# Performance work log

Hardware: AMD Instinct MI355X
Metric: run time of the kernel (lower is better)

The kernel has to match this reference:

```python
import jax, jax.numpy as jnp
import numpy as np
import math

D_MODEL = 1024
N_HEADS = 16
D_K = D_MODEL // N_HEADS


def setup_inputs() -> dict:
    key = jax.random.key(0)
    ks = jax.random.split(key, 12)
    B, S, D = 4, 2048, D_MODEL
    scale = 1.0 / math.sqrt(D)
    inp = {
        "q": jax.random.normal(ks[0], (B, S, D), jnp.float32),
        "k": jax.random.normal(ks[1], (B, S, D), jnp.float32),
        "v": jax.random.normal(ks[2], (B, S, D), jnp.float32),
        "w_q": jax.random.normal(ks[3], (D, D), jnp.float32) * scale,
        "b_q": jnp.zeros((D,), jnp.float32),
        "w_k": jax.random.normal(ks[4], (D, D), jnp.float32) * scale,
        "b_k": jnp.zeros((D,), jnp.float32),
        "w_v": jax.random.normal(ks[5], (D, D), jnp.float32) * scale,
        "b_v": jnp.zeros((D,), jnp.float32),
        "w_o": jax.random.normal(ks[6], (D, D), jnp.float32) * scale,
        "b_o": jnp.zeros((D,), jnp.float32),
        "ln_gamma": jnp.ones((D,), jnp.float32),
        "ln_beta": jnp.zeros((D,), jnp.float32),
    }
    return inp


def reference(q, k, v, w_q, b_q, w_k, b_k, w_v, b_v, w_o, b_o, ln_gamma, ln_beta):
    B, Sq, D = q.shape
    Sk = k.shape[1]
    residual = q
    # Projections (torch Linear: x @ W.T + b); split into heads -> [B, H, S, d_k]
    qh = (q @ w_q.T + b_q).reshape(B, Sq, N_HEADS, D_K).transpose(0, 2, 1, 3)
    kh = (k @ w_k.T + b_k).reshape(B, Sk, N_HEADS, D_K).transpose(0, 2, 1, 3)
    vh = (v @ w_v.T + b_v).reshape(B, Sk, N_HEADS, D_K).transpose(0, 2, 1, 3)
    # Scaled dot-product attention (dropout is identity in eval mode)
    scores = jnp.einsum("bhqd,bhkd->bhqk", qh, kh) / jnp.sqrt(jnp.float32(D_K))
    attn = jax.nn.softmax(scores, axis=-1)  # [B, H, Sq, Sk]
    ctx = jnp.einsum("bhqk,bhkd->bhqd", attn, vh)
    ctx = ctx.transpose(0, 2, 1, 3).reshape(B, Sq, D)
    out = ctx @ w_o.T + b_o
    # Post-LN with residual
    x = out + residual
    mu = jnp.mean(x, axis=-1, keepdims=True)
    var = jnp.var(x, axis=-1, keepdims=True)
    out = (x - mu) / jnp.sqrt(var + 1e-5) * ln_gamma + ln_beta
    return out, attn
```

## Files before the change

kernel.cpp:

```cpp
#include <hip/hip_runtime.h>

#define B_ 4
#define S_ 2048
#define D_ 1024
#define H_ 16
#define DK_ 64
#define M_ (B_ * S_)

typedef __attribute__((ext_vector_type(8))) _Float16 f16x8;
typedef __attribute__((ext_vector_type(4))) _Float16 f16x4;
typedef __attribute__((ext_vector_type(4))) float f32x4;

#define QSCALE 0.18033688011113607f

__device__ __forceinline__ f32x4 mfma16(f16x8 a, f16x8 b, f32x4 c) {
  return __builtin_amdgcn_mfma_f32_16x16x32_f16(a, b, c, 0, 0, 0);
}

__device__ __forceinline__ void gl2lds(const _Float16* g, _Float16* l) {
  __builtin_amdgcn_global_load_lds(
      (const __attribute__((address_space(1))) void*)g,
      (__attribute__((address_space(3))) void*)l, 16, 0, 0);
}

#define NW8 (D_ * D_ / 8)
__global__ __launch_bounds__(256) void cvt_w(
    const float* __restrict__ wq, const float* __restrict__ wk,
    const float* __restrict__ wv, const float* __restrict__ wo,
    _Float16* __restrict__ wqh, _Float16* __restrict__ wkh,
    _Float16* __restrict__ wvh, _Float16* __restrict__ woh) {
  const int i = blockIdx.x * 256 + threadIdx.x;
  const int t = i >> 17;
  const int off = i & (NW8 - 1);
  const float* src = t == 0 ? wq : (t == 1 ? wk : (t == 2 ? wv : wo));
  _Float16* dst = t == 0 ? wqh : (t == 1 ? wkh : (t == 2 ? wvh : woh));
  const f32x4 a = *reinterpret_cast<const f32x4*>(&src[(size_t)off * 8]);
  const f32x4 b = *reinterpret_cast<const f32x4*>(&src[(size_t)off * 8 + 4]);
  f16x8 h;
  h[0] = (_Float16)a[0]; h[1] = (_Float16)a[1]; h[2] = (_Float16)a[2]; h[3] = (_Float16)a[3];
  h[4] = (_Float16)b[0]; h[5] = (_Float16)b[1]; h[6] = (_Float16)b[2]; h[7] = (_Float16)b[3];
  *reinterpret_cast<f16x8*>(&dst[(size_t)off * 8]) = h;
}

__global__ __launch_bounds__(256) void gemm_qkv(
    const float* __restrict__ Xq, const float* __restrict__ Xk, const float* __restrict__ Xv,
    const _Float16* __restrict__ Wq, const _Float16* __restrict__ Wk, const _Float16* __restrict__ Wv,
    const float* __restrict__ bq, const float* __restrict__ bk, const float* __restrict__ bv,
    _Float16* __restrict__ Qh, _Float16* __restrict__ Kh, _Float16* __restrict__ Vt) {
  __shared__ _Float16 As[128 * 72];
  __shared__ _Float16 Bs[128 * 64];
  const int third = blockIdx.x >> 9;
  const int bid = blockIdx.x & 511;
  const float* X = third == 0 ? Xq : (third == 1 ? Xk : Xv);
  const _Float16* Bw = third == 0 ? Wq : (third == 1 ? Wk : Wv);
  const float* bias = third == 0 ? bq : (third == 1 ? bk : bv);

  const int t = threadIdx.x;
  const int lane = t & 63;
  const int w = t >> 6;
  const int wr = w >> 1, wc = w & 1;
  const int l15 = lane & 15, g = lane >> 4;
  const int m0 = (bid & 63) * 128;
  const int n0 = (bid >> 6) * 128;

  f32x4 acc[4][4] = {};
  const int srow = lane >> 3;
  const int schk = (lane & 7) * 8;
  const int ar = t >> 4;
  const int ac = (t & 15) * 4;

  for (int kt = 0; kt < 16; ++kt) {
    const int k0 = kt * 64;
#pragma unroll
    for (int u = 0; u < 4; ++u)
      gl2lds(&Bw[(size_t)(n0 + u * 32 + w * 8 + srow) * D_ + k0 + schk], &Bs[u * 2048 + w * 512]);
#pragma unroll
    for (int rg = 0; rg < 8; ++rg) {
      const int r = rg * 16 + ar;
      const f32x4 vv = *reinterpret_cast<const f32x4*>(&X[(size_t)(m0 + r) * D_ + k0 + ac]);
      f16x4 hh;
      hh[0] = (_Float16)vv[0]; hh[1] = (_Float16)vv[1];
      hh[2] = (_Float16)vv[2]; hh[3] = (_Float16)vv[3];
      *reinterpret_cast<f16x4*>(&As[r * 72 + ac]) = hh;
    }
    __syncthreads();
#pragma unroll
    for (int kk = 0; kk < 2; ++kk) {
      f16x8 af[4], bfr[4];
#pragma unroll
      for (int m = 0; m < 4; ++m)
        af[m] = *reinterpret_cast<const f16x8*>(&As[(wr * 64 + m * 16 + l15) * 72 + kk * 32 + 8 * g]);
#pragma unroll
      for (int n = 0; n < 4; ++n)
        bfr[n] = *reinterpret_cast<const f16x8*>(&Bs[(wc * 64 + n * 16 + l15) * 64 + kk * 32 + 8 * g]);
#pragma unroll
      for (int m = 0; m < 4; ++m)
#pragma unroll
        for (int n = 0; n < 4; ++n)
          acc[m][n] = mfma16(af[m], bfr[n], acc[m][n]);
    }
    __syncthreads();
  }

  if (third < 2) {
    _Float16* Y = third == 0 ? Qh : Kh;
    const float scl = third == 0 ? QSCALE : 1.0f;
#pragma unroll
    for (int m = 0; m < 4; ++m)
#pragma unroll
      for (int n = 0; n < 4; ++n)
#pragma unroll
        for (int i = 0; i < 4; ++i) {
          const int R = m0 + wr * 64 + m * 16 + 4 * g + i;
          const int C = n0 + wc * 64 + n * 16 + l15;
          Y[(size_t)R * D_ + C] = (_Float16)((acc[m][n][i] + bias[C]) * scl);
        }
  } else {
#pragma unroll
    for (int m = 0; m < 4; ++m)
#pragma unroll
      for (int n = 0; n < 4; ++n) {
        const int R0 = m0 + wr * 64 + m * 16 + 4 * g;
        const int C = n0 + wc * 64 + n * 16 + l15;
        const int b = R0 >> 11, s0 = R0 & (S_ - 1);
        const int h = C >> 6, dk = C & (DK_ - 1);
        f16x4 hv;
#pragma unroll
        for (int i = 0; i < 4; ++i) hv[i] = (_Float16)(acc[m][n][i] + bias[C]);
        *reinterpret_cast<f16x4*>(&Vt[((size_t)((b * H_ + h) * DK_ + dk)) * S_ + s0]) = hv;
      }
  }
}

__global__ __launch_bounds__(256) void gemm_out(const _Float16* __restrict__ A,
                                                const _Float16* __restrict__ Bw,
                                                const float* __restrict__ bias,
                                                float* __restrict__ out) {
  __shared__ _Float16 As[128 * 64];
  __shared__ _Float16 Bs[128 * 64];
  const int t = threadIdx.x;
  const int lane = t & 63;
  const int w = t >> 6;
  const int wr = w >> 1, wc = w & 1;
  const int l15 = lane & 15, g = lane >> 4;
  const int m0 = (blockIdx.x & 63) * 128;
  const int n0 = (blockIdx.x >> 6) * 128;

  f32x4 acc[4][4] = {};
  const int srow = lane >> 3;
  const int schk = (lane & 7) * 8;

  for (int kt = 0; kt < 16; ++kt) {
    const int k0 = kt * 64;
#pragma unroll
    for (int u = 0; u < 4; ++u) {
      const int r = u * 32 + w * 8 + srow;
      gl2lds(&A[(size_t)(m0 + r) * D_ + k0 + schk], &As[u * 2048 + w * 512]);
      gl2lds(&Bw[(size_t)(n0 + r) * D_ + k0 + schk], &Bs[u * 2048 + w * 512]);
    }
    __syncthreads();
#pragma unroll
    for (int kk = 0; kk < 2; ++kk) {
      f16x8 af[4], bfr[4];
#pragma unroll
      for (int m = 0; m < 4; ++m)
        af[m] = *reinterpret_cast<const f16x8*>(&As[(wr * 64 + m * 16 + l15) * 64 + kk * 32 + 8 * g]);
#pragma unroll
      for (int n = 0; n < 4; ++n)
        bfr[n] = *reinterpret_cast<const f16x8*>(&Bs[(wc * 64 + n * 16 + l15) * 64 + kk * 32 + 8 * g]);
#pragma unroll
      for (int m = 0; m < 4; ++m)
#pragma unroll
        for (int n = 0; n < 4; ++n)
          acc[m][n] = mfma16(af[m], bfr[n], acc[m][n]);
    }
    __syncthreads();
  }

#pragma unroll
  for (int m = 0; m < 4; ++m)
#pragma unroll
    for (int n = 0; n < 4; ++n)
#pragma unroll
      for (int i = 0; i < 4; ++i) {
        const int R = m0 + wr * 64 + m * 16 + 4 * g + i;
        const int C = n0 + wc * 64 + n * 16 + l15;
        out[(size_t)R * D_ + C] = acc[m][n][i] + bias[C];
      }
}

__global__ __launch_bounds__(256) void attn_pass1(const _Float16* __restrict__ Qh,
                                                  const _Float16* __restrict__ Kh,
                                                  float* __restrict__ lbuf) {
  __shared__ float red[4][64];
  const int t = threadIdx.x;
  const int lane = t & 63;
  const int w = t >> 6;
  const int l15 = lane & 15, g = lane >> 4;
  const int qc = blockIdx.x & 31;
  const int bh = blockIdx.x >> 5;
  const int b = bh >> 4, h = bh & 15;
  const int q0 = qc * 64;
  const _Float16* Qp = Qh + (size_t)b * S_ * D_ + h * DK_;
  const _Float16* Kp = Kh + (size_t)b * S_ * D_ + h * DK_;

  f16x8 qa[4][2];
#pragma unroll
  for (int mr = 0; mr < 4; ++mr)
#pragma unroll
    for (int kk = 0; kk < 2; ++kk)
      qa[mr][kk] = *reinterpret_cast<const f16x8*>(&Qp[(size_t)(q0 + mr * 16 + l15) * D_ + kk * 32 + 8 * g]);

  float l[4][4] = {};
  const int cbeg = w * (S_ / 4), cend = cbeg + (S_ / 4);
  f16x8 kb0 = *reinterpret_cast<const f16x8*>(&Kp[(size_t)(cbeg + l15) * D_ + 8 * g]);
  f16x8 kb1 = *reinterpret_cast<const f16x8*>(&Kp[(size_t)(cbeg + l15) * D_ + 32 + 8 * g]);
  for (int c0 = cbeg; c0 < cend; c0 += 16) {
    const int cn = (c0 + 16 < cend) ? c0 + 16 : cbeg;
    const f16x8 nb0 = *reinterpret_cast<const f16x8*>(&Kp[(size_t)(cn + l15) * D_ + 8 * g]);
    const f16x8 nb1 = *reinterpret_cast<const f16x8*>(&Kp[(size_t)(cn + l15) * D_ + 32 + 8 * g]);
#pragma unroll
    for (int mr = 0; mr < 4; ++mr) {
      f32x4 sc = {};
      sc = mfma16(qa[mr][0], kb0, sc);
      sc = mfma16(qa[mr][1], kb1, sc);
#pragma unroll
      for (int i = 0; i < 4; ++i) l[mr][i] += exp2f(sc[i]);
    }
    kb0 = nb0; kb1 = nb1;
  }
#pragma unroll
  for (int mask = 1; mask < 16; mask <<= 1)
#pragma unroll
    for (int mr = 0; mr < 4; ++mr)
#pragma unroll
      for (int i = 0; i < 4; ++i) l[mr][i] += __shfl_xor(l[mr][i], mask, 64);
  if (l15 == 0)
#pragma unroll
    for (int mr = 0; mr < 4; ++mr)
#pragma unroll
      for (int i = 0; i < 4; ++i) red[w][mr * 16 + 4 * g + i] = l[mr][i];
  __syncthreads();
  if (t < 64)
    lbuf[(size_t)bh * S_ + q0 + t] = red[0][t] + red[1][t] + red[2][t] + red[3][t];
}

__global__ __launch_bounds__(256) void attn_pass2(const _Float16* __restrict__ Qh,
                                                  const _Float16* __restrict__ Kh,
                                                  const _Float16* __restrict__ Vt,
                                                  const float* __restrict__ lbuf,
                                                  float* __restrict__ attn,
                                                  _Float16* __restrict__ ctx) {
  __shared__ float Ps[4][32 * 36];
  const int t = threadIdx.x;
  const int lane = t & 63;
  const int w = t >> 6;
  const int l15 = lane & 15, g = lane >> 4;
  const int qc = blockIdx.x & 15;
  const int bh = blockIdx.x >> 4;
  const int b = bh >> 4, h = bh & 15;
  const int q0 = qc * 128 + w * 32;
  const _Float16* Qp = Qh + (size_t)b * S_ * D_ + h * DK_;
  const _Float16* Kp = Kh + (size_t)b * S_ * D_ + h * DK_;
  const _Float16* Vp = Vt + (size_t)bh * DK_ * S_;

  f16x8 qa[2][2];
#pragma unroll
  for (int mr = 0; mr < 2; ++mr)
#pragma unroll
    for (int kk = 0; kk < 2; ++kk)
      qa[mr][kk] = *reinterpret_cast<const f16x8*>(&Qp[(size_t)(q0 + mr * 16 + l15) * D_ + kk * 32 + 8 * g]);

  float il[2][4];
#pragma unroll
  for (int mr = 0; mr < 2; ++mr)
#pragma unroll
    for (int i = 0; i < 4; ++i)
      il[mr][i] = 1.0f / lbuf[(size_t)bh * S_ + q0 + mr * 16 + 4 * g + i];

  f32x4 accv[2][4] = {};
  float* Pw = Ps[w];
  const int sr = lane >> 3;
  const int sc4 = (lane & 7) * 4;

#pragma unroll 2
  for (int c0 = 0; c0 < S_; c0 += 32) {
#pragma unroll
    for (int ct = 0; ct < 2; ++ct) {
      const f16x8 kb0 = *reinterpret_cast<const f16x8*>(&Kp[(size_t)(c0 + ct * 16 + l15) * D_ + 8 * g]);
      const f16x8 kb1 = *reinterpret_cast<const f16x8*>(&Kp[(size_t)(c0 + ct * 16 + l15) * D_ + 32 + 8 * g]);
#pragma unroll
      for (int mr = 0; mr < 2; ++mr) {
        f32x4 sc = {};
        sc = mfma16(qa[mr][0], kb0, sc);
        sc = mfma16(qa[mr][1], kb1, sc);
#pragma unroll
        for (int i = 0; i < 4; ++i)
          Pw[(mr * 16 + 4 * g + i) * 36 + ct * 16 + l15] = exp2f(sc[i]) * il[mr][i];
      }
    }
#pragma unroll
    for (int j = 0; j < 4; ++j) {
      const int r = sr + 8 * j;
      const f32x4 pv = *reinterpret_cast<const f32x4*>(&Pw[r * 36 + sc4]);
      __builtin_nontemporal_store(pv,
          reinterpret_cast<f32x4*>(&attn[((size_t)bh * S_ + q0 + r) * S_ + c0 + sc4]));
    }
#pragma unroll
    for (int mr = 0; mr < 2; ++mr) {
      const f32x4 p0 = *reinterpret_cast<const f32x4*>(&Pw[(mr * 16 + l15) * 36 + 8 * g]);
      const f32x4 p1 = *reinterpret_cast<const f32x4*>(&Pw[(mr * 16 + l15) * 36 + 8 * g + 4]);
      f16x8 pa;
#pragma unroll
      for (int j = 0; j < 4; ++j) { pa[j] = (_Float16)p0[j]; pa[4 + j] = (_Float16)p1[j]; }
#pragma unroll
      for (int n = 0; n < 4; ++n) {
        const f16x8 vb = *reinterpret_cast<const f16x8*>(&Vp[(size_t)(n * 16 + l15) * S_ + c0 + 8 * g]);
        accv[mr][n] = mfma16(pa, vb, accv[mr][n]);
      }
    }
  }
#pragma unroll
  for (int mr = 0; mr < 2; ++mr)
#pragma unroll
    for (int n = 0; n < 4; ++n)
#pragma unroll
      for (int i = 0; i < 4; ++i) {
        const int row = q0 + mr * 16 + 4 * g + i;
        ctx[((size_t)(b * S_ + row)) * D_ + h * DK_ + n * 16 + l15] = (_Float16)accv[mr][n][i];
      }
}

__global__ __launch_bounds__(256) void ln_kernel(float* __restrict__ out,
                                                 const float* __restrict__ resid,
                                                 const float* __restrict__ gamma,
                                                 const float* __restrict__ beta) {
  const int t = threadIdx.x;
  const int lane = t & 63, w = t >> 6;
  const int row = blockIdx.x * 4 + w;
  const size_t rb = (size_t)row * D_;
  f32x4 x[4];
  float s = 0.f, s2 = 0.f;
#pragma unroll
  for (int c = 0; c < 4; ++c) {
    const int off = c * 256 + lane * 4;
    const f32x4 o = *reinterpret_cast<const f32x4*>(&out[rb + off]);
    const f32x4 r = *reinterpret_cast<const f32x4*>(&resid[rb + off]);
    x[c] = o + r;
#pragma unroll
    for (int j = 0; j < 4; ++j) { s += x[c][j]; s2 += x[c][j] * x[c][j]; }
  }
#pragma unroll
  for (int mask = 1; mask < 64; mask <<= 1) {
    s += __shfl_xor(s, mask, 64);
    s2 += __shfl_xor(s2, mask, 64);
  }
  const float mu = s * (1.0f / D_);
  const float var = s2 * (1.0f / D_) - mu * mu;
  const float rstd = rsqrtf(var + 1e-5f);
#pragma unroll
  for (int c = 0; c < 4; ++c) {
    const int off = c * 256 + lane * 4;
    const f32x4 gm = *reinterpret_cast<const f32x4*>(&gamma[off]);
    const f32x4 bt = *reinterpret_cast<const f32x4*>(&beta[off]);
    f32x4 y;
#pragma unroll
    for (int j = 0; j < 4; ++j) y[j] = (x[c][j] - mu) * rstd * gm[j] + bt[j];
    *reinterpret_cast<f32x4*>(&out[rb + off]) = y;
  }
}

extern "C" void kernel_launch(void* const* d_in, const int* in_sizes, int n_in,
                              void* d_out, int out_size, void* d_ws, size_t ws_size,
                              hipStream_t stream) {
  (void)in_sizes; (void)n_in; (void)out_size; (void)ws_size;
  const float* q    = (const float*)d_in[0];
  const float* k    = (const float*)d_in[1];
  const float* v    = (const float*)d_in[2];
  const float* w_q  = (const float*)d_in[3];
  const float* b_q  = (const float*)d_in[4];
  const float* w_k  = (const float*)d_in[5];
  const float* b_k  = (const float*)d_in[6];
  const float* w_v  = (const float*)d_in[7];
  const float* b_v  = (const float*)d_in[8];
  const float* w_o  = (const float*)d_in[9];
  const float* b_o  = (const float*)d_in[10];
  const float* ln_g = (const float*)d_in[11];
  const float* ln_b = (const float*)d_in[12];

  char* ws = (char*)d_ws;
  _Float16* wq_h = (_Float16*)(ws + ((size_t)0 << 20));
  _Float16* wk_h = (_Float16*)(ws + ((size_t)2 << 20));
  _Float16* wv_h = (_Float16*)(ws + ((size_t)4 << 20));
  _Float16* wo_h = (_Float16*)(ws + ((size_t)6 << 20));
  _Float16* Qh   = (_Float16*)(ws + ((size_t)8 << 20));
  _Float16* Kh   = (_Float16*)(ws + ((size_t)26 << 20));
  _Float16* Vt   = (_Float16*)(ws + ((size_t)44 << 20));
  _Float16* ctx  = (_Float16*)(ws + ((size_t)62 << 20));
  float*    lbuf = (float*)(ws + ((size_t)80 << 20));

  float* out_f = (float*)d_out;
  float* attn_f = out_f + (size_t)M_ * D_;

  cvt_w<<<4 * NW8 / 256, 256, 0, stream>>>(w_q, w_k, w_v, w_o, wq_h, wk_h, wv_h, wo_h);

  gemm_qkv<<<1536, 256, 0, stream>>>(q, k, v, wq_h, wk_h, wv_h, b_q, b_k, b_v, Qh, Kh, Vt);

  attn_pass1<<<B_ * H_ * (S_ / 64), 256, 0, stream>>>(Qh, Kh, lbuf);
  attn_pass2<<<B_ * H_ * (S_ / 128), 256, 0, stream>>>(Qh, Kh, Vt, lbuf, attn_f, ctx);

  gemm_out<<<512, 256, 0, stream>>>(ctx, wo_h, b_o, out_f);
  ln_kernel<<<M_ / 4, 256, 0, stream>>>(out_f, q, ln_g, ln_b);
}
```

Baseline: 500.0 us.

## Double-buffer QKV GEMM tiles and remap attention blocks across XCDs

The QKV projection GEMM now uses double-buffered LDS tiles. The next K-tile's weights are prefetched via global_load_lds and its activations are loaded into registers while the current tile's MFMAs run, and the single sync per iteration replaces two. The attention pass kernels also permute blockIdx so consecutive (batch, head, query-chunk) tiles are grouped per XCD, which should improve L2 reuse of K/V. The double buffering doubles LDS use and adds live registers, and launch bounds now request 2 blocks per CU.

```diff
diff --git a/kernel.cpp b/kernel.cpp
--- a/kernel.cpp
+++ b/kernel.cpp
@@ -42,13 +42,13 @@
   *reinterpret_cast<f16x8*>(&dst[(size_t)off * 8]) = h;
 }
 
-__global__ __launch_bounds__(256) void gemm_qkv(
+__global__ __launch_bounds__(256, 2) void gemm_qkv(
     const float* __restrict__ Xq, const float* __restrict__ Xk, const float* __restrict__ Xv,
     const _Float16* __restrict__ Wq, const _Float16* __restrict__ Wk, const _Float16* __restrict__ Wv,
     const float* __restrict__ bq, const float* __restrict__ bk, const float* __restrict__ bv,
     _Float16* __restrict__ Qh, _Float16* __restrict__ Kh, _Float16* __restrict__ Vt) {
-  __shared__ _Float16 As[128 * 72];
-  __shared__ _Float16 Bs[128 * 64];
+  __shared__ _Float16 As[2][128 * 72];
+  __shared__ _Float16 Bs[2][128 * 64];
   const int third = blockIdx.x >> 9;
   const int bid = blockIdx.x & 511;
   const float* X = third == 0 ? Xq : (third == 1 ? Xk : Xv);
@@ -69,35 +69,57 @@
   const int ar = t >> 4;
   const int ac = (t & 15) * 4;
 
+  f32x4 av[8];
+
+#pragma unroll
+  for (int u = 0; u < 4; ++u)
+    gl2lds(&Bw[(size_t)(n0 + u * 32 + w * 8 + srow) * D_ + schk], &Bs[0][u * 2048 + w * 512]);
+#pragma unroll
+  for (int rg = 0; rg < 8; ++rg)
+    av[rg] = *reinterpret_cast<const f32x4*>(&X[(size_t)(m0 + rg * 16 + ar) * D_ + ac]);
+#pragma unroll
+  for (int rg = 0; rg < 8; ++rg) {
+    f16x4 hh;
+    hh[0] = (_Float16)av[rg][0]; hh[1] = (_Float16)av[rg][1];
+    hh[2] = (_Float16)av[rg][2]; hh[3] = (_Float16)av[rg][3];
+    *reinterpret_cast<f16x4*>(&As[0][(rg * 16 + ar) * 72 + ac]) = hh;
+  }
+  __syncthreads();
+
   for (int kt = 0; kt < 16; ++kt) {
-    const int k0 = kt * 64;
-#pragma unroll
-    for (int u = 0; u < 4; ++u)
-      gl2lds(&Bw[(size_t)(n0 + u * 32 + w * 8 + srow) * D_ + k0 + schk], &Bs[u * 2048 + w * 512]);
-#pragma unroll
-    for (int rg = 0; rg < 8; ++rg) {
-      const int r = rg * 16 + ar;
-      const f32x4 vv = *reinterpret_cast<const f32x4*>(&X[(size_t)(m0 + r) * D_ + k0 + ac]);
-      f16x4 hh;
-      hh[0] = (_Float16)vv[0]; hh[1] = (_Float16)vv[1];
-      hh[2] = (_Float16)vv[2]; hh[3] = (_Float16)vv[3];
-      *reinterpret_cast<f16x4*>(&As[r * 72 + ac]) = hh;
-    }
-    __syncthreads();
+    const int cur = kt & 1;
+    if (kt < 15) {
+      const int k1 = (kt + 1) * 64;
+#pragma unroll
+      for (int u = 0; u < 4; ++u)
+        gl2lds(&Bw[(size_t)(n0 + u * 32 + w * 8 + srow) * D_ + k1 + schk], &Bs[cur ^ 1][u * 2048 + w * 512]);
+#pragma unroll
+      for (int rg = 0; rg < 8; ++rg)
+        av[rg] = *reinterpret_cast<const f32x4*>(&X[(size_t)(m0 + rg * 16 + ar) * D_ + k1 + ac]);
+    }
 #pragma unroll
     for (int kk = 0; kk < 2; ++kk) {
       f16x8 af[4], bfr[4];
 #pragma unroll
       for (int m = 0; m < 4; ++m)
-        af[m] = *reinterpret_cast<const f16x8*>(&As[(wr * 64 + m * 16 + l15) * 72 + kk * 32 + 8 * g]);
+        af[m] = *reinterpret_cast<const f16x8*>(&As[cur][(wr * 64 + m * 16 + l15) * 72 + kk * 32 + 8 * g]);
 #pragma unroll
       for (int n = 0; n < 4; ++n)
-        bfr[n] = *reinterpret_cast<const f16x8*>(&Bs[(wc * 64 + n * 16 + l15) * 64 + kk * 32 + 8 * g]);
+        bfr[n] = *reinterpret_cast<const f16x8*>(&Bs[cur][(wc * 64 + n * 16 + l15) * 64 + kk * 32 + 8 * g]);
 #pragma unroll
       for (int m = 0; m < 4; ++m)
 #pragma unroll
         for (int n = 0; n < 4; ++n)
           acc[m][n] = mfma16(af[m], bfr[n], acc[m][n]);
+    }
+    if (kt < 15) {
+#pragma unroll
+      for (int rg = 0; rg < 8; ++rg) {
+        f16x4 hh;
+        hh[0] = (_Float16)av[rg][0]; hh[1] = (_Float16)av[rg][1];
+        hh[2] = (_Float16)av[rg][2]; hh[3] = (_Float16)av[rg][3];
+        *reinterpret_cast<f16x4*>(&As[cur ^ 1][(rg * 16 + ar) * 72 + ac]) = hh;
+      }
     }
     __syncthreads();
   }
@@ -197,8 +219,9 @@
   const int lane = t & 63;
   const int w = t >> 6;
   const int l15 = lane & 15, g = lane >> 4;
-  const int qc = blockIdx.x & 31;
-  const int bh = blockIdx.x >> 5;
+  const int bid = (blockIdx.x & 7) * 256 + (blockIdx.x >> 3);
+  const int qc = bid & 31;
+  const int bh = bid >> 5;
   const int b = bh >> 4, h = bh & 15;
   const int q0 = qc * 64;
   const _Float16* Qp = Qh + (size_t)b * S_ * D_ + h * DK_;
@@ -256,8 +279,9 @@
   const int lane = t & 63;
   const int w = t >> 6;
   const int l15 = lane & 15, g = lane >> 4;
-  const int qc = blockIdx.x & 15;
-  const int bh = blockIdx.x >> 4;
+  const int bid = (blockIdx.x & 7) * 128 + (blockIdx.x >> 3);
+  const int qc = bid & 15;
+  const int bh = bid >> 4;
   const int b = bh >> 4, h = bh & 15;
   const int q0 = qc * 128 + w * 32;
   const _Float16* Qp = Qh + (size_t)b * S_ * D_ + h * DK_;
```

Measured after the change: 522.8 us. 4.6% more time.
